# Optimization experiments

Measured on AMD Instinct MI355X. Metric: run time of the kernel, lower is better.

The kernel has to match this reference:

```python
import jax, jax.numpy as jnp
import numpy as np

N, B, L, E = 64, 128, 4096, 16
BN_EPS = 1e-5


def setup_inputs() -> dict:
    key = jax.random.key(0)
    ks = jax.random.split(key, 6)
    feat = jax.random.normal(ks[0], (N, B, L), dtype=jnp.float32)
    # Glorot-ish scaled linear weights
    Wl = jax.random.normal(ks[1], (L, E), dtype=jnp.float32) * (1.0 / np.sqrt(L))
    Wr = jax.random.normal(ks[2], (L, E), dtype=jnp.float32) * (1.0 / np.sqrt(L))
    Wm = jax.random.normal(ks[3], (L, L), dtype=jnp.float32) * (1.0 / np.sqrt(L))
    return {
        "feat": feat,
        "Wl": Wl, "bl": jnp.zeros((E,), jnp.float32),
        "Wr": Wr, "br": jnp.zeros((E,), jnp.float32),
        "Wm": Wm, "bm": jnp.zeros((L,), jnp.float32),
        "gamma": jnp.ones((N * N,), jnp.float32),
        "beta": jnp.zeros((N * N,), jnp.float32),
        "bias": jnp.zeros((L,), jnp.float32),
    }


def reference(feat, Wl, bl, Wr, br, Wm, bm, gamma, beta, bias):
    # feat: (N, B, L) node time series
    # Attention projections (lookup_l / lookup_r): Linear(L -> E)
    att_l = feat @ Wl + bl                      # (N, B, E) on src nodes
    att_r = feat @ Wr + br                      # (N, B, E) on dst nodes

    # Feature extractor: MLP Linear(L, L) + ReLU over the time axis
    out = jax.nn.relu(jnp.einsum('nbl,kl->nbk', feat, Wm) + bm)   # (N, B, L)

    # Edge scores on the complete graph: e[d, s, b] = att_l[src=s] . att_r[dst=d]
    e = jnp.einsum('sbe,dbe->dsb', att_l, att_r)                  # (Nd, Ns, B)

    # BatchNorm1d over N*N edge channels (training-mode batch statistics)
    ef = e.reshape(N * N, B)
    mu = ef.mean(axis=1, keepdims=True)
    var = ef.var(axis=1, keepdims=True)
    ef = gamma[:, None] * (ef - mu) * jax.lax.rsqrt(var + BN_EPS) + beta[:, None]
    e = ef.reshape(N, N, B)

    # edge_softmax: normalize over incoming edges (src axis) per destination node
    w = jax.nn.softmax(e, axis=1)                                  # (Nd, Ns, B)

    # Weighted neighbor aggregation + bias
    rst = jnp.einsum('dsb,sbl->dbl', w, out) + bias                # (N, B, L)
    return rst
```

## Files before the change

kernel.cpp:

```cpp
#include <hip/hip_runtime.h>
#include <stdint.h>
#include <stddef.h>

#define NN 64
#define BB 128
#define LL 4096
#define EE 16

typedef __attribute__((ext_vector_type(4))) float f32x4;
typedef __attribute__((ext_vector_type(8))) short short8;
typedef __attribute__((ext_vector_type(4))) unsigned short u16x4;

__device__ __forceinline__ unsigned short f2bf(float f) {
  union { float f; unsigned u; } v; v.f = f;
  unsigned r = v.u + 0x7FFFu + ((v.u >> 16) & 1u);
  return (unsigned short)(r >> 16);
}
__device__ __forceinline__ float bf2f(unsigned short h) {
  union { unsigned u; float f; } v; v.u = ((unsigned)h) << 16;
  return v.f;
}
__device__ __forceinline__ void gload16(const void* g, void* l) {
  __builtin_amdgcn_global_load_lds((const __attribute__((address_space(1))) void*)g,
                                   (__attribute__((address_space(3))) void*)l,
                                   16, 0, 0);
}

__global__ __launch_bounds__(256) void k_cvt(const float* __restrict__ src,
                                             unsigned short* __restrict__ dst, int n4) {
  int i = blockIdx.x * 256 + threadIdx.x;
  int stride = gridDim.x * 256;
  for (; i < n4; i += stride) {
    f32x4 v = ((const f32x4*)src)[i];
    u16x4 o;
    o[0] = f2bf(v[0]); o[1] = f2bf(v[1]); o[2] = f2bf(v[2]); o[3] = f2bf(v[3]);
    ((u16x4*)dst)[i] = o;
  }
}

__global__ __launch_bounds__(256) void k_att(const float* __restrict__ feat,
    const float* __restrict__ Wl, const float* __restrict__ bl,
    const float* __restrict__ Wr, const float* __restrict__ br,
    unsigned short* __restrict__ feat_bf,
    float* __restrict__ att_l, float* __restrict__ att_r) {
  __shared__ __align__(16) float wlds[128][36];
  __shared__ __align__(16) float flds[8][132];
  __shared__ __align__(16) float red[4][64][4];
  int t = threadIdx.x;
  int rowBase = blockIdx.x * 8;
  int lane = t & 63, wave = t >> 6;
  int row = lane >> 3, eg = lane & 7;
  float acc0 = 0.f, acc1 = 0.f, acc2 = 0.f, acc3 = 0.f;
  for (int kc = 0; kc < 32; ++kc) {
    int k0 = kc * 128;
    __syncthreads();
    for (int i = t; i < 512; i += 256) {
      int kk = i >> 2, ee = (i & 3) * 4;
      *(f32x4*)&wlds[kk][ee]      = *(const f32x4*)&Wl[(size_t)(k0 + kk) * 16 + ee];
      *(f32x4*)&wlds[kk][16 + ee] = *(const f32x4*)&Wr[(size_t)(k0 + kk) * 16 + ee];
    }
    {
      int rr = t >> 5, kk = (t & 31) * 4;
      size_t gi = (size_t)(rowBase + rr) * LL + k0 + kk;
      f32x4 v = *(const f32x4*)&feat[gi];
      *(f32x4*)&flds[rr][kk] = v;
      u16x4 o; o[0] = f2bf(v[0]); o[1] = f2bf(v[1]); o[2] = f2bf(v[2]); o[3] = f2bf(v[3]);
      *(u16x4*)&feat_bf[gi] = o;
    }
    __syncthreads();
    int kb = wave * 32;
    #pragma unroll
    for (int k2 = 0; k2 < 32; ++k2) {
      int k = kb + k2;
      float fv = flds[row][k];
      f32x4 wv = *(const f32x4*)&wlds[k][eg * 4];
      acc0 += fv * wv[0]; acc1 += fv * wv[1]; acc2 += fv * wv[2]; acc3 += fv * wv[3];
    }
  }
  red[wave][lane][0] = acc0; red[wave][lane][1] = acc1;
  red[wave][lane][2] = acc2; red[wave][lane][3] = acc3;
  __syncthreads();
  if (t < 64) {
    f32x4 s = *(f32x4*)&red[0][t][0];
    #pragma unroll
    for (int w2 = 1; w2 < 4; ++w2) {
      f32x4 v = *(f32x4*)&red[w2][t][0];
      s[0] += v[0]; s[1] += v[1]; s[2] += v[2]; s[3] += v[3];
    }
    int r = rowBase + (t >> 3);
    int e0 = (t & 7) * 4;
    #pragma unroll
    for (int q = 0; q < 4; ++q) {
      int e = e0 + q;
      if (e < 16) att_l[(size_t)r * 16 + e]        = s[q] + bl[e];
      else        att_r[(size_t)r * 16 + (e - 16)] = s[q] + br[e - 16];
    }
  }
}

__global__ __launch_bounds__(256) void k_edge(const float* __restrict__ att_l,
    const float* __restrict__ att_r, const float* __restrict__ gamma,
    const float* __restrict__ beta, float* __restrict__ w_t) {
  __shared__ __align__(16) float attr[BB][20];
  __shared__ float el[NN][BB + 1];
  __shared__ float part[NN][4][2];
  __shared__ float sc[NN], sh[NN];
  int d = blockIdx.x, t = threadIdx.x;
  for (int i = t; i < 512; i += 256) {
    int b = i >> 2, e = (i & 3) * 4;
    *(f32x4*)&attr[b][e] = *(const f32x4*)&att_r[((size_t)d * BB + b) * 16 + e];
  }
  __syncthreads();
  for (int v = t; v < NN * BB; v += 256) {
    int s = v >> 7, b = v & 127;
    const float* al = &att_l[((size_t)s * BB + b) * 16];
    float acc = 0.f;
    #pragma unroll
    for (int e4 = 0; e4 < 4; ++e4) {
      f32x4 a = *(const f32x4*)&al[e4 * 4];
      f32x4 r = *(const f32x4*)&attr[b][e4 * 4];
      acc += a[0] * r[0] + a[1] * r[1] + a[2] * r[2] + a[3] * r[3];
    }
    el[s][b] = acc;
  }
  __syncthreads();
  {
    int s = t >> 2, q = t & 3;
    float sum = 0.f, ss = 0.f;
    for (int b = q * 32; b < q * 32 + 32; ++b) { float x = el[s][b]; sum += x; ss += x * x; }
    part[s][q][0] = sum; part[s][q][1] = ss;
  }
  __syncthreads();
  if (t < 64) {
    float sum = 0.f, ss = 0.f;
    #pragma unroll
    for (int q = 0; q < 4; ++q) { sum += part[t][q][0]; ss += part[t][q][1]; }
    float mu = sum * (1.f / 128.f);
    float var = ss * (1.f / 128.f) - mu * mu;
    int c = d * 64 + t;
    float a = gamma[c] * rsqrtf(fmaxf(var, 0.f) + 1e-5f);
    sc[t] = a; sh[t] = beta[c] - mu * a;
  }
  __syncthreads();
  if (t < 128) {
    int b = t;
    float y[64];
    float m = -1e30f;
    #pragma unroll
    for (int s = 0; s < 64; ++s) { y[s] = sc[s] * el[s][b] + sh[s]; m = fmaxf(m, y[s]); }
    float sum = 0.f;
    #pragma unroll
    for (int s = 0; s < 64; ++s) { y[s] = __expf(y[s] - m); sum += y[s]; }
    float inv = 1.f / sum;
    float* wp = &w_t[((size_t)b * 64 + d) * 64];
    #pragma unroll
    for (int s4 = 0; s4 < 16; ++s4) {
      f32x4 o;
      o[0] = y[s4 * 4 + 0] * inv; o[1] = y[s4 * 4 + 1] * inv;
      o[2] = y[s4 * 4 + 2] * inv; o[3] = y[s4 * 4 + 3] * inv;
      *(f32x4*)&wp[s4 * 4] = o;
    }
  }
}

#define LDS_A 0
#define LDS_B 65536
#define BAR   do { __builtin_amdgcn_sched_barrier(0); __builtin_amdgcn_s_barrier(); __builtin_amdgcn_sched_barrier(0); } while (0)
#define LGKM0 do { asm volatile("s_waitcnt lgkmcnt(0)" ::: "memory"); __builtin_amdgcn_sched_barrier(0); } while (0)
#define VM6   asm volatile("s_waitcnt vmcnt(6)" ::: "memory")
#define VM4   asm volatile("s_waitcnt vmcnt(4)" ::: "memory")
#define VM0   asm volatile("s_waitcnt vmcnt(0)" ::: "memory")
#define PRIO1 __builtin_amdgcn_s_setprio(1)
#define PRIO0 __builtin_amdgcn_s_setprio(0)
#define MFMA(a, b, c) __builtin_amdgcn_mfma_f32_16x16x32_bf16((a), (b), (c), 0, 0, 0)
#define STAGE2(g0, g1, ldsoff) do { \
    gload16((g0), lds_raw + (ldsoff) + tid16); \
    gload16((g1), lds_raw + (ldsoff) + 8192 + tid16); } while (0)

__global__ __launch_bounds__(512, 2) void k_gemm8(const unsigned short* __restrict__ A,
    const unsigned short* __restrict__ Bm, const float* __restrict__ bm,
    unsigned short* __restrict__ C) {
  __shared__ __align__(16) char lds_raw[131072];
  const int tid = threadIdx.x;
  const int lane = tid & 63, wave = tid >> 6;
  const int wm = wave >> 2, wn = wave & 3;
  int bid = blockIdx.x;
  int swz = (bid & 7) * 64 + (bid >> 3);
  int tM = swz >> 4, tN = swz & 15;
  const size_t rowBase = (size_t)tM * 256, colBase = (size_t)tN * 256;
  const int tid16 = tid * 16;
  const int o0 = tid16, o1 = tid16 + 8192;
  const int r0s = (o0 & 1023) >> 6, r1s = (o1 & 1023) >> 6;
  const int row0 = (o0 >> 10) * 16 + r0s, row1 = (o1 >> 10) * 16 + r1s;
  const int col0 = (((o0 >> 4) & 3) ^ ((r0s >> 3) << 1)) * 8;
  const int col1 = (((o1 >> 4) & 3) ^ ((r1s >> 3) << 1)) * 8;
  const unsigned short* aR0 = A  + (rowBase + row0) * LL + col0;
  const unsigned short* aR1 = A  + (rowBase + row1) * LL + col1;
  const unsigned short* bR0 = Bm + (colBase + row0) * LL + col0;
  const unsigned short* bR1 = Bm + (colBase + row1) * LL + col1;
  const int rr = lane & 15, gg = lane >> 4;
  const int rdswz = rr * 64 + ((gg ^ ((rr >> 3) << 1)) << 4);
  f32x4 acc[8][4] = {};
  STAGE2(aR0 +  0, aR1 +  0, LDS_A + 0);
  STAGE2(bR0 +  0, bR1 +  0, LDS_B + 0);
  STAGE2(aR0 + 32, aR1 + 32, LDS_A + 16384);
  STAGE2(bR0 + 32, bR1 + 32, LDS_B + 16384);
  VM4;
  STAGE2(aR0 + 64, aR1 + 64, LDS_A + 32768);
  STAGE2(bR0 + 64, bR1 + 64, LDS_B + 32768);
  STAGE2(aR0 + 96, aR1 + 96, LDS_A + 32768 + 16384);
  VM6;
  BAR;
  #pragma unroll 2
  for (int t = 0; t < 64; ++t) {
    const int d = t & 1;
    const char* pA = lds_raw + LDS_A + d * 32768 + wm * 8192 + rdswz;
    const char* pB = lds_raw + LDS_B + d * 32768 + wn * 4096 + rdswz;
    short8 ar[8], bx, by;
    #pragma unroll
    for (int mi = 0; mi < 8; ++mi) ar[mi] = *(const short8*)(pA + mi * 1024);
    bx = *(const short8*)(pB + 0);
    by = *(const short8*)(pB + 1024);
    if (t <= 62) { size_t kc = (size_t)(t + 1) * 64 + 32;
      STAGE2(bR0 + kc, bR1 + kc, LDS_B + ((t + 1) & 1) * 32768 + 16384); }
    BAR; LGKM0; PRIO1;
    #pragma unroll
    for (int mi = 0; mi < 8; ++mi) {
      acc[mi][0] = MFMA(ar[mi], bx, acc[mi][0]);
      acc[mi][1] = MFMA(ar[mi], by, acc[mi][1]);
    }
    PRIO0; BAR;
    bx = *(const short8*)(pB + 2048);
    by = *(const short8*)(pB + 3072);
    if (t <= 61) { size_t kc = (size_t)(t + 2) * 64;
      STAGE2(aR0 + kc, aR1 + kc, LDS_A + d * 32768); }
    BAR; LGKM0; PRIO1;
    #pragma unroll
    for (int mi = 0; mi < 8; ++mi) {
      acc[mi][2] = MFMA(ar[mi], bx, acc[mi][2]);
      acc[mi][3] = MFMA(ar[mi], by, acc[mi][3]);
    }
    PRIO0; BAR;
    #pragma unroll
    for (int mi = 0; mi < 8; ++mi) ar[mi] = *(const short8*)(pA + 16384 + mi * 1024);
    bx = *(const short8*)(pB + 16384 + 2048);
    by = *(const short8*)(pB + 16384 + 3072);
    if (t <= 61) { size_t kc = (size_t)(t + 2) * 64;
      STAGE2(bR0 + kc, bR1 + kc, LDS_B + d * 32768); }
    BAR; LGKM0; PRIO1;
    #pragma unroll
    for (int mi = 0; mi < 8; ++mi) {
      acc[mi][2] = MFMA(ar[mi], bx, acc[mi][2]);
      acc[mi][3] = MFMA(ar[mi], by, acc[mi][3]);
    }
    PRIO0; BAR;
    bx = *(const short8*)(pB + 16384);
    by = *(const short8*)(pB + 16384 + 1024);
    if (t <= 61) { size_t kc = (size_t)(t + 2) * 64 + 32;
      STAGE2(aR0 + kc, aR1 + kc, LDS_A + d * 32768 + 16384); }
    BAR; LGKM0; PRIO1;
    #pragma unroll
    for (int mi = 0; mi < 8; ++mi) {
      acc[mi][0] = MFMA(ar[mi], bx, acc[mi][0]);
      acc[mi][1] = MFMA(ar[mi], by, acc[mi][1]);
    }
    PRIO0;
    if (t < 62) { VM6; } else { VM0; }
    BAR;
  }
  const int co = lane & 15, ro4 = (lane >> 4) * 4;
  #pragma unroll
  for (int mig = 0; mig < 8; ++mig) {
    size_t r0 = rowBase + (size_t)wm * 128 + mig * 16 + ro4;
    #pragma unroll
    for (int nj = 0; nj < 4; ++nj) {
      size_t c = colBase + (size_t)wn * 64 + nj * 16 + co;
      float bc = bm[c];
      #pragma unroll
      for (int j = 0; j < 4; ++j) {
        float v = acc[mig][nj][j] + bc;
        v = fmaxf(v, 0.f);
        C[(r0 + j) * LL + c] = f2bf(v);
      }
    }
  }
}

__global__ __launch_bounds__(256) void k_agg(const float* __restrict__ w_t,
    const unsigned short* __restrict__ outb, const float* __restrict__ bias,
    float* __restrict__ rst) {
  __shared__ __align__(16) float wl[64][64];
  int b = blockIdx.y;
  int t = threadIdx.x;
  int l = blockIdx.x * 256 + t;
  {
    const f32x4* src = (const f32x4*)&w_t[(size_t)b * 4096];
    f32x4* dstp = (f32x4*)&wl[0][0];
    for (int i = t; i < 1024; i += 256) dstp[i] = src[i];
  }
  __syncthreads();
  float o[64];
  #pragma unroll
  for (int s = 0; s < 64; ++s) o[s] = bf2f(outb[((size_t)s * BB + b) * LL + l]);
  float bs = bias[l];
  #pragma unroll 2
  for (int d = 0; d < 64; ++d) {
    float acc = 0.f;
    #pragma unroll
    for (int s4 = 0; s4 < 16; ++s4) {
      f32x4 wv = *(const f32x4*)&wl[d][s4 * 4];
      acc += wv[0] * o[s4 * 4 + 0] + wv[1] * o[s4 * 4 + 1]
           + wv[2] * o[s4 * 4 + 2] + wv[3] * o[s4 * 4 + 3];
    }
    rst[((size_t)d * BB + b) * LL + l] = acc + bs;
  }
}

extern "C" void kernel_launch(void* const* d_in, const int* in_sizes, int n_in,
                              void* d_out, int out_size, void* d_ws, size_t ws_size,
                              hipStream_t stream) {
  (void)in_sizes; (void)n_in; (void)out_size; (void)ws_size;
  const float* feat  = (const float*)d_in[0];
  const float* Wl    = (const float*)d_in[1];
  const float* bl    = (const float*)d_in[2];
  const float* Wr    = (const float*)d_in[3];
  const float* br    = (const float*)d_in[4];
  const float* Wm    = (const float*)d_in[5];
  const float* bm    = (const float*)d_in[6];
  const float* gamma = (const float*)d_in[7];
  const float* beta  = (const float*)d_in[8];
  const float* bias  = (const float*)d_in[9];
  char* ws = (char*)d_ws;
  unsigned short* feat_bf = (unsigned short*)(ws);
  unsigned short* wm_bf   = (unsigned short*)(ws + 67108864ull);
  unsigned short* out_bf  = (unsigned short*)(ws + 100663296ull);
  float* att_l = (float*)(ws + 167772160ull);
  float* att_r = (float*)(ws + 168296448ull);
  float* w_t   = (float*)(ws + 168820736ull);
  float* rst = (float*)d_out;

  k_cvt<<<dim3(2048), dim3(256), 0, stream>>>(Wm, wm_bf, (LL * LL) / 4);
  k_att<<<dim3(1024), dim3(256), 0, stream>>>(feat, Wl, bl, Wr, br, feat_bf, att_l, att_r);
  k_edge<<<dim3(64), dim3(256), 0, stream>>>(att_l, att_r, gamma, beta, w_t);
  k_gemm8<<<dim3(512), dim3(512), 0, stream>>>(feat_bf, wm_bf, bm, out_bf);
  k_agg<<<dim3(16, 128), dim3(256), 0, stream>>>(w_t, out_bf, bias, rst);
}
```

Before: 442.2 us.

## Process two columns per thread in aggregation and relax GEMM barrier scheduling

```diff
diff --git a/kernel.cpp b/kernel.cpp
--- a/kernel.cpp
+++ b/kernel.cpp
@@ -8,6 +8,7 @@
 #define EE 16
 
 typedef __attribute__((ext_vector_type(4))) float f32x4;
+typedef __attribute__((ext_vector_type(2))) float f32x2;
 typedef __attribute__((ext_vector_type(8))) short short8;
 typedef __attribute__((ext_vector_type(4))) unsigned short u16x4;
 
@@ -165,8 +166,9 @@
 
 #define LDS_A 0
 #define LDS_B 65536
-#define BAR   do { __builtin_amdgcn_sched_barrier(0); __builtin_amdgcn_s_barrier(); __builtin_amdgcn_sched_barrier(0); } while (0)
-#define LGKM0 do { asm volatile("s_waitcnt lgkmcnt(0)" ::: "memory"); __builtin_amdgcn_sched_barrier(0); } while (0)
+#define BAR   __builtin_amdgcn_s_barrier()
+#define LGKM0 asm volatile("s_waitcnt lgkmcnt(0)" ::: "memory")
+#define LGKM8 asm volatile("s_waitcnt lgkmcnt(8)" ::: "memory")
 #define VM6   asm volatile("s_waitcnt vmcnt(6)" ::: "memory")
 #define VM4   asm volatile("s_waitcnt vmcnt(4)" ::: "memory")
 #define VM0   asm volatile("s_waitcnt vmcnt(0)" ::: "memory")
@@ -223,6 +225,7 @@
     by = *(const short8*)(pB + 1024);
     if (t <= 62) { size_t kc = (size_t)(t + 1) * 64 + 32;
       STAGE2(bR0 + kc, bR1 + kc, LDS_B + ((t + 1) & 1) * 32768 + 16384); }
+    LGKM8;
     BAR; LGKM0; PRIO1;
     #pragma unroll
     for (int mi = 0; mi < 8; ++mi) {
@@ -247,6 +250,7 @@
     by = *(const short8*)(pB + 16384 + 3072);
     if (t <= 61) { size_t kc = (size_t)(t + 2) * 64;
       STAGE2(bR0 + kc, bR1 + kc, LDS_B + d * 32768); }
+    LGKM8;
     BAR; LGKM0; PRIO1;
     #pragma unroll
     for (int mi = 0; mi < 8; ++mi) {
@@ -286,33 +290,37 @@
   }
 }
 
-__global__ __launch_bounds__(256) void k_agg(const float* __restrict__ w_t,
+__global__ __launch_bounds__(256) void k_agg2(const float* __restrict__ w_t,
     const unsigned short* __restrict__ outb, const float* __restrict__ bias,
     float* __restrict__ rst) {
-  __shared__ __align__(16) float wl[64][64];
   int b = blockIdx.y;
   int t = threadIdx.x;
-  int l = blockIdx.x * 256 + t;
-  {
-    const f32x4* src = (const f32x4*)&w_t[(size_t)b * 4096];
-    f32x4* dstp = (f32x4*)&wl[0][0];
-    for (int i = t; i < 1024; i += 256) dstp[i] = src[i];
-  }
-  __syncthreads();
-  float o[64];
+  int l0 = blockIdx.x * 512 + t * 2;
+  float oA[64], oB[64];
   #pragma unroll
-  for (int s = 0; s < 64; ++s) o[s] = bf2f(outb[((size_t)s * BB + b) * LL + l]);
-  float bs = bias[l];
+  for (int s = 0; s < 64; ++s) {
+    unsigned u = *(const unsigned*)&outb[((size_t)s * BB + b) * LL + l0];
+    oA[s] = bf2f((unsigned short)(u & 0xFFFF));
+    oB[s] = bf2f((unsigned short)(u >> 16));
+  }
+  const float* wb = w_t + (size_t)b * 4096;
+  float bs0 = bias[l0], bs1 = bias[l0 + 1];
   #pragma unroll 2
   for (int d = 0; d < 64; ++d) {
-    float acc = 0.f;
-    #pragma unroll
-    for (int s4 = 0; s4 < 16; ++s4) {
-      f32x4 wv = *(const f32x4*)&wl[d][s4 * 4];
-      acc += wv[0] * o[s4 * 4 + 0] + wv[1] * o[s4 * 4 + 1]
-           + wv[2] * o[s4 * 4 + 2] + wv[3] * o[s4 * 4 + 3];
-    }
-    rst[((size_t)d * BB + b) * LL + l] = acc + bs;
+    const float* wr = wb + d * 64;
+    float a0 = 0.f, a1 = 0.f;
+    #pragma unroll
+    for (int q = 0; q < 16; ++q) {
+      f32x4 wq = *(const f32x4*)&wr[q * 4];
+      #pragma unroll
+      for (int j = 0; j < 4; ++j) {
+        float wv = wq[j];
+        a0 += wv * oA[q * 4 + j];
+        a1 += wv * oB[q * 4 + j];
+      }
+    }
+    f32x2 o; o[0] = a0 + bs0; o[1] = a1 + bs1;
+    *(f32x2*)&rst[((size_t)d * BB + b) * LL + l0] = o;
   }
 }
 
@@ -343,5 +351,5 @@
   k_att<<<dim3(1024), dim3(256), 0, stream>>>(feat, Wl, bl, Wr, br, feat_bf, att_l, att_r);
   k_edge<<<dim3(64), dim3(256), 0, stream>>>(att_l, att_r, gamma, beta, w_t);
   k_gemm8<<<dim3(512), dim3(512), 0, stream>>>(feat_bf, wm_bf, bm, out_bf);
-  k_agg<<<dim3(16, 128), dim3(256), 0, stream>>>(w_t, out_bf, bias, rst);
-}
+  k_agg2<<<dim3(8, 128), dim3(256), 0, stream>>>(w_t, out_bf, bias, rst);
+}
```

Result: no change. 447.9 us (+1.3%).
